# Optimization experiments

Measured on AMD Instinct MI355X. Metric: run time of the kernel, lower is better.

The kernel has to match this reference:

```python
import jax, jax.numpy as jnp
from jax import lax
import numpy as np

N_GROUP = 1024   # number of FPS centroids
N_SAMPLE = 32    # neighbors per ball query
RADIUS = 0.2
BN_EPS = 1e-5    # torch BatchNorm2d default, training-mode batch stats
MLP = [64, 64, 128]
IN_CH = 6        # 3 relative xyz + 3 point features


def setup_inputs() -> dict:
    key = jax.random.key(0)
    ks = jax.random.split(key, 8)
    B, N = 16, 4096
    out = {
        "xyz": jax.random.uniform(ks[0], (B, N, 3), dtype=jnp.float32),
        "point_feature": jax.random.normal(ks[1], (B, N, 3), dtype=jnp.float32),
    }
    last = IN_CH
    for li, oc in enumerate(MLP):
        out[f"w{li}"] = jax.random.normal(ks[2 + li], (oc, last), dtype=jnp.float32) / np.float32(np.sqrt(last))
        out[f"b{li}"] = jnp.zeros((oc,), jnp.float32)
        out[f"g{li}"] = jnp.ones((oc,), jnp.float32)
        out[f"be{li}"] = jnp.zeros((oc,), jnp.float32)
        last = oc
    return out


def _fps(xyz, n_group):
    # Farthest point sampling. xyz: [B, N, 3] -> idx [B, n_group]
    B, N, _ = xyz.shape

    def step(carry, _):
        dist, farthest = carry                      # [B,N], [B]
        centroid = jnp.take_along_axis(xyz, farthest[:, None, None], axis=1)  # [B,1,3]
        d = jnp.sum((xyz - centroid) ** 2, -1)      # [B,N]
        dist = jnp.minimum(dist, d)
        nxt = jnp.argmax(dist, -1).astype(jnp.int32)
        return (dist, nxt), farthest

    init = (jnp.full((B, N), 1e10, xyz.dtype), jnp.zeros((B,), jnp.int32))
    _, idxs = lax.scan(step, init, None, length=n_group)
    return idxs.T                                    # [B, n_group]


def _ball_query(xyz, new_xyz, radius, n_sample):
    # xyz: [B,N,3], new_xyz: [B,S,3] -> idx [B,S,n_sample]
    B, N, _ = xyz.shape
    sqr = jnp.sum((new_xyz[:, :, None, :] - xyz[:, None, :, :]) ** 2, -1)  # [B,S,N]
    idx = jnp.where(sqr > radius * radius, N, jnp.arange(N, dtype=jnp.int32))
    idx = jnp.sort(idx, axis=-1)[:, :, :n_sample]    # closest-index fill like torch impl
    first = idx[:, :, :1]
    return jnp.where(idx == N, first, idx)


def reference(xyz, point_feature, w0, b0, g0, be0, w1, b1, g1, be1, w2, b2, g2, be2):
    B = xyz.shape[0]
    fps_idx = _fps(xyz, N_GROUP)                     # [B,S]
    bi = jnp.arange(B)[:, None]
    new_xyz = xyz[bi, fps_idx]                       # [B,S,3]

    idx = _ball_query(xyz, new_xyz, RADIUS, N_SAMPLE)  # [B,S,K]
    bii = jnp.arange(B)[:, None, None]
    grouped_xyz = xyz[bii, idx] - new_xyz[:, :, None, :]   # [B,S,K,3] centered
    grouped_feat = point_feature[bii, idx]                 # [B,S,K,3]
    x = jnp.concatenate([grouped_xyz, grouped_feat], -1)   # [B,S,K,6]

    # 1x1 Conv2d == per-point linear; BN over all dims but channel (training stats)
    for w, b, g, be in ((w0, b0, g0, be0), (w1, b1, g1, be1), (w2, b2, g2, be2)):
        x = jnp.einsum('bskc,oc->bsko', x, w) + b
        mu = x.mean((0, 1, 2))
        var = x.var((0, 1, 2))
        x = g * (x - mu) * lax.rsqrt(var + BN_EPS) + be
        x = jax.nn.relu(x)

    new_feature = x.max(axis=2)                      # max over n_sample -> [B,S,128]
    return new_xyz, new_feature
```

## Files before the change

### kernel.cpp

```cpp
#include <hip/hip_runtime.h>

constexpr int BATCH = 16;
constexpr int NPT   = 4096;
constexpr int NGRP  = 1024;
constexpr int NSMP  = 32;
constexpr int NPTS  = BATCH * NGRP * NSMP;
constexpr int PBLK  = 4096;
constexpr int NG    = BATCH * NGRP;

__device__ __forceinline__ float sqd(float dx, float dy, float dz) {
  return __fadd_rn(__fadd_rn(__fmul_rn(dx, dx), __fmul_rn(dy, dy)), __fmul_rn(dz, dz));
}

template <int CTRL, int RM>
__device__ __forceinline__ unsigned long long dpp_lvl(unsigned long long P) {
  const int lo = (int)(unsigned int)P;
  const int hi = (int)(unsigned int)(P >> 32);
  const int tlo = __builtin_amdgcn_update_dpp(lo, lo, CTRL, RM, 0xF, false);
  const int thi = __builtin_amdgcn_update_dpp(hi, hi, CTRL, RM, 0xF, false);
  const unsigned long long T =
      ((unsigned long long)(unsigned int)thi << 32) | (unsigned int)tlo;
  return (T > P) ? T : P;
}

__global__ __launch_bounds__(256) void fps_kernel(const float* __restrict__ xyz,
                                                  float* __restrict__ out) {
  __shared__ float sx[NPT], sy[NPT], sz[NPT];
  __shared__ unsigned int ex[2][5][4];
  const int b = blockIdx.x;
  const int t = threadIdx.x;
  const float* src = xyz + (size_t)b * NPT * 3;
  for (int i = t; i < NPT; i += 256) {
    sx[i] = src[i * 3 + 0];
    sy[i] = src[i * 3 + 1];
    sz[i] = src[i * 3 + 2];
  }
  __syncthreads();
  float px[16], py[16], pz[16], dist[16];
  #pragma unroll
  for (int j = 0; j < 16; ++j) {
    const int p = j * 256 + t;
    px[j] = sx[p]; py[j] = sy[p]; pz[j] = sz[p];
    dist[j] = 1e10f;
  }
  const int w = t >> 6;
  float cx = sx[0], cy = sy[0], cz = sz[0];
  float* outx = out + (size_t)b * NGRP * 3;
  for (int step = 0; step < NGRP; ++step) {
    if (t == 0) {
      outx[step * 3 + 0] = cx;
      outx[step * 3 + 1] = cy;
      outx[step * 3 + 2] = cz;
    }
    float bestd = -1.0f; int bestj = 0;
    #pragma unroll
    for (int j = 0; j < 16; ++j) {
      float d = sqd(px[j] - cx, py[j] - cy, pz[j] - cz);
      d = fminf(dist[j], d);
      dist[j] = d;
      if (d > bestd) { bestd = d; bestj = j; }
    }
    const int myidx = bestj * 256 + t;
    const unsigned long long myP =
        ((unsigned long long)__float_as_uint(bestd) << 32) |
        (unsigned long long)(unsigned int)~myidx;
    const float mx = sx[myidx], my_ = sy[myidx], mz = sz[myidx];
    unsigned long long P = myP;
    P = dpp_lvl<0xB1, 0xF>(P);
    P = dpp_lvl<0x4E, 0xF>(P);
    P = dpp_lvl<0x141, 0xF>(P);
    P = dpp_lvl<0x140, 0xF>(P);
    P = dpp_lvl<0x142, 0xA>(P);
    P = dpp_lvl<0x143, 0xC>(P);
    const unsigned int flo = (unsigned int)__builtin_amdgcn_readlane((int)(unsigned int)P, 63);
    const unsigned int fhi =
        (unsigned int)__builtin_amdgcn_readlane((int)(unsigned int)(P >> 32), 63);
    const unsigned long long PF = ((unsigned long long)fhi << 32) | flo;
    const int pb = step & 1;
    if (myP == PF) {
      ex[pb][0][w] = fhi;
      ex[pb][1][w] = flo;
      ex[pb][2][w] = __float_as_uint(mx);
      ex[pb][3][w] = __float_as_uint(my_);
      ex[pb][4][w] = __float_as_uint(mz);
    }
    __syncthreads();
    const unsigned int* e = &ex[pb][0][0];
    unsigned long long best = ((unsigned long long)e[0] << 32) | e[4];
    cx = __uint_as_float(e[8]);
    cy = __uint_as_float(e[12]);
    cz = __uint_as_float(e[16]);
    #pragma unroll
    for (int k = 1; k < 4; ++k) {
      const unsigned long long pk_ = ((unsigned long long)e[k] << 32) | e[4 + k];
      if (pk_ > best) {
        best = pk_;
        cx = __uint_as_float(e[8 + k]);
        cy = __uint_as_float(e[12 + k]);
        cz = __uint_as_float(e[16 + k]);
      }
    }
  }
}

__global__ __launch_bounds__(256) void ballq_kernel(const float* __restrict__ xyz,
                                                    const float* __restrict__ out,
                                                    int* __restrict__ idxg) {
  __shared__ float sx[NPT], sy[NPT], sz[NPT];
  const int b = blockIdx.x >> 4;
  const int sub = blockIdx.x & 15;
  const float* src = xyz + (size_t)b * NPT * 3;
  for (int i = threadIdx.x; i < NPT; i += 256) {
    sx[i] = src[i * 3 + 0];
    sy[i] = src[i * 3 + 1];
    sz[i] = src[i * 3 + 2];
  }
  __syncthreads();
  const int lane = threadIdx.x & 63;
  const int w = threadIdx.x >> 6;
  const float R2 = __fmul_rn(0.2f, 0.2f);
  for (int gi = 0; gi < 16; ++gi) {
    const int s = sub * 64 + w * 16 + gi;
    const float* c = out + ((size_t)b * NGRP + s) * 3;
    const float nx = c[0], ny = c[1], nz = c[2];
    int* og = idxg + ((size_t)b * NGRP + s) * NSMP;
    int cnt = 0, firstP = -1;
    for (int base = 0; base < NPT; base += 64) {
      const int p = base + lane;
      const float dsq = sqd(nx - sx[p], ny - sy[p], nz - sz[p]);
      const bool inr = (dsq <= R2);
      unsigned long long m = __ballot(inr);
      if (firstP < 0 && m) firstP = base + (int)__builtin_ctzll(m);
      const int rank = (int)__popcll(m & ((1ull << lane) - 1ull));
      if (inr) {
        const int pos = cnt + rank;
        if (pos < NSMP) og[pos] = p;
      }
      cnt += (int)__popcll(m);
      if (cnt >= NSMP) break;
    }
    if (cnt < NSMP) {
      for (int pos = cnt + lane; pos < NSMP; pos += 64) og[pos] = firstP;
    }
  }
}

__global__ void transpose_w3(const float* __restrict__ w3, float* __restrict__ w3t) {
  const int i = blockIdx.x * 256 + threadIdx.x;
  if (i < 128 * 64) {
    const int o = i >> 6, c = i & 63;
    w3t[c * 128 + o] = w3[i];
  }
}

__device__ __forceinline__ void gather6(const float* __restrict__ xyz, const float* __restrict__ pf,
                                        const float* __restrict__ nxyz, const int* __restrict__ idxg,
                                        int tid, float in[6]) {
  const int g = tid >> 5;
  const int b = g >> 10;
  const int i = idxg[tid];
  const float* P = xyz + ((size_t)b * NPT + i) * 3;
  const float* C = nxyz + (size_t)g * 3;
  in[0] = P[0] - C[0];
  in[1] = P[1] - C[1];
  in[2] = P[2] - C[2];
  const float* F = pf + ((size_t)b * NPT + i) * 3;
  in[3] = F[0]; in[4] = F[1]; in[5] = F[2];
}

__device__ __forceinline__ void layer1h(const float in[6], const float* __restrict__ w1,
                                        const float* __restrict__ b1, const float* __restrict__ ss1,
                                        float h1[64]) {
  #pragma unroll
  for (int o = 0; o < 64; ++o) {
    float a = b1[o];
    #pragma unroll
    for (int cc = 0; cc < 6; ++cc) a = fmaf(in[cc], w1[o * 6 + cc], a);
    h1[o] = fmaxf(0.0f, fmaf(a, ss1[o], ss1[64 + o]));
  }
}

__device__ __forceinline__ void zb_stats64(const float* zb, float* __restrict__ part,
                                           int chbase, int nch, int t, int blk) {
  const int c = t >> 1, h = t & 1;
  const float* row = zb + c * 129 + h * 64;
  float s = 0.0f, q = 0.0f;
  for (int i = 0; i < 64; ++i) {
    const float v = row[i];
    s += v;
    q = fmaf(v, v, q);
  }
  s += __shfl_xor(s, 1);
  q += __shfl_xor(q, 1);
  if (h == 0) {
    part[(size_t)(chbase + c) * PBLK + blk]       = s;
    part[(size_t)(nch + chbase + c) * PBLK + blk] = q;
  }
}

__device__ __forceinline__ void zb_stats_mm(const float* zb, float* __restrict__ part,
                                            float* __restrict__ pmax, float* __restrict__ pmin,
                                            int chbase, int nch, int t, int blk) {
  const int c = t >> 1, h = t & 1;
  const float* row = zb + c * 129 + h * 64;
  float s = 0.0f, q = 0.0f;
  float mx0 = -3.4e38f, mn0 = 3.4e38f, mx1 = -3.4e38f, mn1 = 3.4e38f;
  for (int i = 0; i < 32; ++i) {
    const float v = row[i];
    s += v; q = fmaf(v, v, q);
    mx0 = fmaxf(mx0, v); mn0 = fminf(mn0, v);
  }
  for (int i = 32; i < 64; ++i) {
    const float v = row[i];
    s += v; q = fmaf(v, v, q);
    mx1 = fmaxf(mx1, v); mn1 = fminf(mn1, v);
  }
  s += __shfl_xor(s, 1);
  q += __shfl_xor(q, 1);
  if (h == 0) {
    part[(size_t)(chbase + c) * PBLK + blk]       = s;
    part[(size_t)(nch + chbase + c) * PBLK + blk] = q;
  }
  const size_t g0 = (size_t)blk * 4 + 2 * h;
  pmax[g0 * 128 + chbase + c]       = mx0;
  pmax[(g0 + 1) * 128 + chbase + c] = mx1;
  pmin[g0 * 128 + chbase + c]       = mn0;
  pmin[(g0 + 1) * 128 + chbase + c] = mn1;
}

__global__ __launch_bounds__(128) void pass1_kernel(const float* __restrict__ xyz, const float* __restrict__ pf,
                                                    const float* __restrict__ nxyz, const int* __restrict__ idxg,
                                                    const float* __restrict__ w1, const float* __restrict__ b1,
                                                    float* __restrict__ part) {
  __shared__ float zb[64 * 129];
  const int t = threadIdx.x;
  const int tid = blockIdx.x * 128 + t;
  float in[6];
  gather6(xyz, pf, nxyz, idxg, tid, in);
  for (int o = 0; o < 64; ++o) {
    float a = b1[o];
    #pragma unroll
    for (int cc = 0; cc < 6; ++cc) a = fmaf(in[cc], w1[o * 6 + cc], a);
    zb[o * 129 + t] = a;
  }
  __syncthreads();
  zb_stats64(zb, part, 0, 64, t, blockIdx.x);
}

__global__ __launch_bounds__(256) void reduce_kernel(const float* __restrict__ part, int nblk, int nch,
                                                     const float* __restrict__ g, const float* __restrict__ be,
                                                     float* __restrict__ ss) {
  const int c = blockIdx.x;
  const int t = threadIdx.x;
  double s = 0.0, q = 0.0;
  for (int i = t; i < nblk; i += 256) {
    s += (double)part[(size_t)c * nblk + i];
    q += (double)part[(size_t)(nch + c) * nblk + i];
  }
  #pragma unroll
  for (int off = 1; off < 64; off <<= 1) {
    s += __shfl_xor(s, off);
    q += __shfl_xor(q, off);
  }
  __shared__ double ls[4], lq[4];
  const int lane = t & 63, w = t >> 6;
  if (lane == 0) { ls[w] = s; lq[w] = q; }
  __syncthreads();
  if (t == 0) {
    const double S = ls[0] + ls[1] + ls[2] + ls[3];
    const double Q = lq[0] + lq[1] + lq[2] + lq[3];
    const double n = (double)NPTS;
    const double mu = S / n;
    const double var = Q / n - mu * mu;
    const double inv = 1.0 / sqrt(var + 1e-5);
    ss[c]       = (float)((double)g[c] * inv);
    ss[nch + c] = (float)((double)be[c] - (double)g[c] * mu * inv);
  }
}

__global__ __launch_bounds__(128) void pass2_kernel(const float* __restrict__ xyz, const float* __restrict__ pf,
                                                    const float* __restrict__ nxyz, const int* __restrict__ idxg,
                                                    const float* __restrict__ w1, const float* __restrict__ b1,
                                                    const float* __restrict__ ss1,
                                                    const float* __restrict__ w2, const float* __restrict__ b2,
                                                    float* __restrict__ part) {
  __shared__ float zb[64 * 129];
  const int t = threadIdx.x;
  const int tid = blockIdx.x * 128 + t;
  float in[6];
  gather6(xyz, pf, nxyz, idxg, tid, in);
  float h1[64];
  layer1h(in, w1, b1, ss1, h1);
  for (int o = 0; o < 64; ++o) {
    float a = b2[o];
    #pragma unroll
    for (int cc = 0; cc < 64; ++cc) a = fmaf(h1[cc], w2[o * 64 + cc], a);
    zb[o * 129 + t] = a;
  }
  __syncthreads();
  zb_stats64(zb, part, 0, 64, t, blockIdx.x);
}

__device__ __forceinline__ void compute_z3(const float* __restrict__ xyz, const float* __restrict__ pf,
                                           const float* __restrict__ nxyz, const int* __restrict__ idxg,
                                           const float* __restrict__ w1, const float* __restrict__ b1,
                                           const float* __restrict__ ss1,
                                           const float* __restrict__ w2, const float* __restrict__ b2,
                                           const float* __restrict__ ss2,
                                           const float* __restrict__ w3t, const float* __restrict__ b3,
                                           float* shm, int t, int tid, float acc[128]) {
  float in[6];
  gather6(xyz, pf, nxyz, idxg, tid, in);
  float h1[64];
  layer1h(in, w1, b1, ss1, h1);
  float* hrow = shm + t * 65;
  for (int o = 0; o < 64; ++o) {
    float a = b2[o];
    #pragma unroll
    for (int cc = 0; cc < 64; ++cc) a = fmaf(h1[cc], w2[o * 64 + cc], a);
    hrow[o] = fmaxf(0.0f, fmaf(a, ss2[o], ss2[64 + o]));
  }
  #pragma unroll
  for (int o = 0; o < 128; ++o) acc[o] = b3[o];
  for (int cc = 0; cc < 64; ++cc) {
    const float hc = hrow[cc];
    const float* wrow = w3t + cc * 128;
    #pragma unroll
    for (int o = 0; o < 128; ++o) acc[o] = fmaf(hc, wrow[o], acc[o]);
  }
}

__global__ __launch_bounds__(128) void pass3_kernel(const float* __restrict__ xyz, const float* __restrict__ pf,
                                                    const float* __restrict__ nxyz, const int* __restrict__ idxg,
                                                    const float* __restrict__ w1, const float* __restrict__ b1,
                                                    const float* __restrict__ ss1,
                                                    const float* __restrict__ w2, const float* __restrict__ b2,
                                                    const float* __restrict__ ss2,
                                                    const float* __restrict__ w3t, const float* __restrict__ b3,
                                                    float* __restrict__ part,
                                                    float* __restrict__ pmax, float* __restrict__ pmin) {
  __shared__ float shm[8320];
  const int t = threadIdx.x;
  const int tid = blockIdx.x * 128 + t;
  float acc[128];
  compute_z3(xyz, pf, nxyz, idxg, w1, b1, ss1, w2, b2, ss2, w3t, b3, shm, t, tid, acc);
  __syncthreads();
  #pragma unroll
  for (int o = 0; o < 64; ++o) shm[o * 129 + t] = acc[o];
  __syncthreads();
  if (pmax) zb_stats_mm(shm, part, pmax, pmin, 0, 128, t, blockIdx.x);
  else      zb_stats64(shm, part, 0, 128, t, blockIdx.x);
  __syncthreads();
  #pragma unroll
  for (int o = 0; o < 64; ++o) shm[o * 129 + t] = acc[64 + o];
  __syncthreads();
  if (pmax) zb_stats_mm(shm, part, pmax, pmin, 64, 128, t, blockIdx.x);
  else      zb_stats64(shm, part, 64, 128, t, blockIdx.x);
}

__global__ __launch_bounds__(256) void pass4f_kernel(const float* __restrict__ pmax,
                                                     const float* __restrict__ pmin,
                                                     const float* __restrict__ ss3,
                                                     float* __restrict__ outF) {
  const int i = blockIdx.x * 256 + threadIdx.x;
  const int c = i & 127;
  const float a = ss3[c], bb = ss3[128 + c];
  const float z = (a >= 0.0f) ? pmax[i] : pmin[i];
  outF[i] = fmaxf(0.0f, fmaf(z, a, bb));
}

__global__ __launch_bounds__(128) void pass4_kernel(const float* __restrict__ xyz, const float* __restrict__ pf,
                                                    const float* __restrict__ nxyz, const int* __restrict__ idxg,
                                                    const float* __restrict__ w1, const float* __restrict__ b1,
                                                    const float* __restrict__ ss1,
                                                    const float* __restrict__ w2, const float* __restrict__ b2,
                                                    const float* __restrict__ ss2,
                                                    const float* __restrict__ w3t, const float* __restrict__ b3,
                                                    const float* __restrict__ ss3,
                                                    float* __restrict__ outF) {
  __shared__ float shm[8320];
  const int t = threadIdx.x;
  const int tid = blockIdx.x * 128 + t;
  float acc[128];
  compute_z3(xyz, pf, nxyz, idxg, w1, b1, ss1, w2, b2, ss2, w3t, b3, shm, t, tid, acc);
  #pragma unroll
  for (int o = 0; o < 128; ++o)
    acc[o] = fmaxf(0.0f, fmaf(acc[o], ss3[o], ss3[128 + o]));
  __syncthreads();
  const int c4 = t & 63, gp = t >> 6;
  #pragma unroll
  for (int o = 0; o < 64; ++o) shm[o * 129 + t] = acc[o];
  __syncthreads();
  #pragma unroll
  for (int gs = 0; gs < 2; ++gs) {
    const int g = gp * 2 + gs;
    const float* row = shm + c4 * 129 + g * 32;
    float m = row[0];
    for (int i = 1; i < 32; ++i) m = fmaxf(m, row[i]);
    outF[((size_t)blockIdx.x * 4 + g) * 128 + c4] = m;
  }
  __syncthreads();
  #pragma unroll
  for (int o = 0; o < 64; ++o) shm[o * 129 + t] = acc[64 + o];
  __syncthreads();
  #pragma unroll
  for (int gs = 0; gs < 2; ++gs) {
    const int g = gp * 2 + gs;
    const float* row = shm + c4 * 129 + g * 32;
    float m = row[0];
    for (int i = 1; i < 32; ++i) m = fmaxf(m, row[i]);
    outF[((size_t)blockIdx.x * 4 + g) * 128 + 64 + c4] = m;
  }
}

extern "C" void kernel_launch(void* const* d_in, const int* in_sizes, int n_in,
                              void* d_out, int out_size, void* d_ws, size_t ws_size,
                              hipStream_t stream) {
  (void)in_sizes; (void)n_in; (void)out_size;
  const float* xyz = (const float*)d_in[0];
  const float* pf  = (const float*)d_in[1];
  const float* w1  = (const float*)d_in[2];
  const float* b1  = (const float*)d_in[3];
  const float* g1  = (const float*)d_in[4];
  const float* be1 = (const float*)d_in[5];
  const float* w2  = (const float*)d_in[6];
  const float* b2  = (const float*)d_in[7];
  const float* g2  = (const float*)d_in[8];
  const float* be2 = (const float*)d_in[9];
  const float* w3  = (const float*)d_in[10];
  const float* b3  = (const float*)d_in[11];
  const float* g3  = (const float*)d_in[12];
  const float* be3 = (const float*)d_in[13];
  float* out = (float*)d_out;

  int*   idxg = (int*)d_ws;
  float* p1   = (float*)((char*)d_ws + (size_t)NPTS * 4);
  float* ss1  = p1 + (size_t)PBLK * 128;
  float* p2   = ss1 + 128;
  float* ss2  = p2 + (size_t)PBLK * 128;
  float* p3   = ss2 + 128;
  float* ss3  = p3 + (size_t)PBLK * 256;
  float* w3t  = ss3 + 256;
  float* pmax = w3t + 8192;
  float* pmin = pmax + (size_t)NG * 128;
  const size_t needed = (size_t)((char*)(pmin + (size_t)NG * 128) - (char*)d_ws);
  const bool fast4 = (ws_size >= needed);

  transpose_w3<<<32, 256, 0, stream>>>(w3, w3t);
  fps_kernel<<<BATCH, 256, 0, stream>>>(xyz, out);
  ballq_kernel<<<BATCH * 16, 256, 0, stream>>>(xyz, out, idxg);
  pass1_kernel<<<PBLK, 128, 0, stream>>>(xyz, pf, out, idxg, w1, b1, p1);
  reduce_kernel<<<64, 256, 0, stream>>>(p1, PBLK, 64, g1, be1, ss1);
  pass2_kernel<<<PBLK, 128, 0, stream>>>(xyz, pf, out, idxg, w1, b1, ss1, w2, b2, p2);
  reduce_kernel<<<64, 256, 0, stream>>>(p2, PBLK, 64, g2, be2, ss2);
  pass3_kernel<<<PBLK, 128, 0, stream>>>(xyz, pf, out, idxg, w1, b1, ss1, w2, b2, ss2, w3t, b3, p3,
                                         fast4 ? pmax : nullptr, fast4 ? pmin : nullptr);
  reduce_kernel<<<128, 256, 0, stream>>>(p3, PBLK, 128, g3, be3, ss3);
  float* outF = out + (size_t)BATCH * NGRP * 3;
  if (fast4) {
    pass4f_kernel<<<(NG * 128) / 256, 256, 0, stream>>>(pmax, pmin, ss3, outF);
  } else {
    pass4_kernel<<<PBLK, 128, 0, stream>>>(xyz, pf, out, idxg, w1, b1, ss1, w2, b2, ss2, w3t, b3, ss3,
                                           outF);
  }
}
```

Before: 1.396 ms.

## Pack two batches per FPS block with 512 threads

The farthest point sampling kernel now processes two batch items per 512-thread block, each half using its own shared-memory point arrays and exchange buffers, and launches half as many blocks. A single __syncthreads now couples both halves at every step, so each batch's serial loop waits on the other. This halves the block count on a kernel that already used only 16 blocks, which seems aimed at per-block or per-CU latency effects, but it also puts two batches on one CU and adds cross-batch barrier coupling.

New measurement: 1.735 ms. 24.3% more time.

```diff
diff --git a/kernel.cpp b/kernel.cpp
--- a/kernel.cpp
+++ b/kernel.cpp
@@ -23,28 +23,29 @@
   return (T > P) ? T : P;
 }
 
-__global__ __launch_bounds__(256) void fps_kernel(const float* __restrict__ xyz,
+__global__ __launch_bounds__(512) void fps_kernel(const float* __restrict__ xyz,
                                                   float* __restrict__ out) {
-  __shared__ float sx[NPT], sy[NPT], sz[NPT];
-  __shared__ unsigned int ex[2][5][4];
-  const int b = blockIdx.x;
-  const int t = threadIdx.x;
+  __shared__ float sx[2][NPT], sy[2][NPT], sz[2][NPT];
+  __shared__ unsigned int ex[2][2][5][4];
+  const int sub = threadIdx.x >> 8;
+  const int t = threadIdx.x & 255;
+  const int b = blockIdx.x * 2 + sub;
   const float* src = xyz + (size_t)b * NPT * 3;
   for (int i = t; i < NPT; i += 256) {
-    sx[i] = src[i * 3 + 0];
-    sy[i] = src[i * 3 + 1];
-    sz[i] = src[i * 3 + 2];
+    sx[sub][i] = src[i * 3 + 0];
+    sy[sub][i] = src[i * 3 + 1];
+    sz[sub][i] = src[i * 3 + 2];
   }
   __syncthreads();
   float px[16], py[16], pz[16], dist[16];
   #pragma unroll
   for (int j = 0; j < 16; ++j) {
     const int p = j * 256 + t;
-    px[j] = sx[p]; py[j] = sy[p]; pz[j] = sz[p];
+    px[j] = sx[sub][p]; py[j] = sy[sub][p]; pz[j] = sz[sub][p];
     dist[j] = 1e10f;
   }
-  const int w = t >> 6;
-  float cx = sx[0], cy = sy[0], cz = sz[0];
+  const int w = (threadIdx.x >> 6) & 3;
+  float cx = sx[sub][0], cy = sy[sub][0], cz = sz[sub][0];
   float* outx = out + (size_t)b * NGRP * 3;
   for (int step = 0; step < NGRP; ++step) {
     if (t == 0) {
@@ -64,7 +65,7 @@
     const unsigned long long myP =
         ((unsigned long long)__float_as_uint(bestd) << 32) |
         (unsigned long long)(unsigned int)~myidx;
-    const float mx = sx[myidx], my_ = sy[myidx], mz = sz[myidx];
+    const float mx = sx[sub][myidx], my_ = sy[sub][myidx], mz = sz[sub][myidx];
     unsigned long long P = myP;
     P = dpp_lvl<0xB1, 0xF>(P);
     P = dpp_lvl<0x4E, 0xF>(P);
@@ -78,14 +79,14 @@
     const unsigned long long PF = ((unsigned long long)fhi << 32) | flo;
     const int pb = step & 1;
     if (myP == PF) {
-      ex[pb][0][w] = fhi;
-      ex[pb][1][w] = flo;
-      ex[pb][2][w] = __float_as_uint(mx);
-      ex[pb][3][w] = __float_as_uint(my_);
-      ex[pb][4][w] = __float_as_uint(mz);
+      ex[sub][pb][0][w] = fhi;
+      ex[sub][pb][1][w] = flo;
+      ex[sub][pb][2][w] = __float_as_uint(mx);
+      ex[sub][pb][3][w] = __float_as_uint(my_);
+      ex[sub][pb][4][w] = __float_as_uint(mz);
     }
     __syncthreads();
-    const unsigned int* e = &ex[pb][0][0];
+    const unsigned int* e = &ex[sub][pb][0][0];
     unsigned long long best = ((unsigned long long)e[0] << 32) | e[4];
     cx = __uint_as_float(e[8]);
     cy = __uint_as_float(e[12]);
@@ -447,7 +448,7 @@
   const bool fast4 = (ws_size >= needed);
 
   transpose_w3<<<32, 256, 0, stream>>>(w3, w3t);
-  fps_kernel<<<BATCH, 256, 0, stream>>>(xyz, out);
+  fps_kernel<<<BATCH / 2, 512, 0, stream>>>(xyz, out);
   ballq_kernel<<<BATCH * 16, 256, 0, stream>>>(xyz, out, idxg);
   pass1_kernel<<<PBLK, 128, 0, stream>>>(xyz, pf, out, idxg, w1, b1, p1);
   reduce_kernel<<<64, 256, 0, stream>>>(p1, PBLK, 64, g1, be1, ss1);
```

## Compute layer-1 BN stats from input moments; tree-reduce FPS argmax

Applied to the files above, without the earlier changes.

Layer-1 batch-norm statistics are now derived analytically from the first and second moments of the 6-channel grouped input (6 sums plus 21 cross products), finalized in double precision with the weights. This replaces materializing 64 channel outputs per point and reducing them. Separately, the FPS per-thread argmax over 16 registers becomes a pairwise tree of selects instead of a serial compare chain, which shortens the per-step dependency chain. Float accumulation of second moments followed by mean subtraction risks cancellation, and the single-block finalize adds a serial reduction over 4096 partials.

After: 1.704 ms. 22.0% more time.

```diff
diff --git a/kernel.cpp b/kernel.cpp
--- a/kernel.cpp
+++ b/kernel.cpp
@@ -52,14 +52,38 @@
       outx[step * 3 + 1] = cy;
       outx[step * 3 + 2] = cz;
     }
-    float bestd = -1.0f; int bestj = 0;
+    float d[16];
     #pragma unroll
     for (int j = 0; j < 16; ++j) {
-      float d = sqd(px[j] - cx, py[j] - cy, pz[j] - cz);
-      d = fminf(dist[j], d);
-      dist[j] = d;
-      if (d > bestd) { bestd = d; bestj = j; }
-    }
+      float dd = sqd(px[j] - cx, py[j] - cy, pz[j] - cz);
+      dd = fminf(dist[j], dd);
+      dist[j] = dd;
+      d[j] = dd;
+    }
+    float v0[8]; int i0[8];
+    #pragma unroll
+    for (int k = 0; k < 8; ++k) {
+      const bool g = d[2 * k + 1] > d[2 * k];
+      v0[k] = g ? d[2 * k + 1] : d[2 * k];
+      i0[k] = g ? 2 * k + 1 : 2 * k;
+    }
+    float v1[4]; int i1[4];
+    #pragma unroll
+    for (int k = 0; k < 4; ++k) {
+      const bool g = v0[2 * k + 1] > v0[2 * k];
+      v1[k] = g ? v0[2 * k + 1] : v0[2 * k];
+      i1[k] = g ? i0[2 * k + 1] : i0[2 * k];
+    }
+    float v2[2]; int i2[2];
+    #pragma unroll
+    for (int k = 0; k < 2; ++k) {
+      const bool g = v1[2 * k + 1] > v1[2 * k];
+      v2[k] = g ? v1[2 * k + 1] : v1[2 * k];
+      i2[k] = g ? i1[2 * k + 1] : i1[2 * k];
+    }
+    const bool gf = v2[1] > v2[0];
+    const float bestd = gf ? v2[1] : v2[0];
+    const int bestj = gf ? i2[1] : i2[0];
     const int myidx = bestj * 256 + t;
     const unsigned long long myP =
         ((unsigned long long)__float_as_uint(bestd) << 32) |
@@ -228,23 +252,80 @@
   pmin[(g0 + 1) * 128 + chbase + c] = mn1;
 }
 
-__global__ __launch_bounds__(128) void pass1_kernel(const float* __restrict__ xyz, const float* __restrict__ pf,
-                                                    const float* __restrict__ nxyz, const int* __restrict__ idxg,
-                                                    const float* __restrict__ w1, const float* __restrict__ b1,
-                                                    float* __restrict__ part) {
-  __shared__ float zb[64 * 129];
-  const int t = threadIdx.x;
-  const int tid = blockIdx.x * 128 + t;
-  float in[6];
-  gather6(xyz, pf, nxyz, idxg, tid, in);
-  for (int o = 0; o < 64; ++o) {
-    float a = b1[o];
-    #pragma unroll
-    for (int cc = 0; cc < 6; ++cc) a = fmaf(in[cc], w1[o * 6 + cc], a);
-    zb[o * 129 + t] = a;
-  }
-  __syncthreads();
-  zb_stats64(zb, part, 0, 64, t, blockIdx.x);
+__global__ __launch_bounds__(256) void mom1_kernel(const float* __restrict__ xyz,
+                                                   const float* __restrict__ pf,
+                                                   const float* __restrict__ nxyz,
+                                                   const int* __restrict__ idxg,
+                                                   float* __restrict__ part) {
+  const int t = threadIdx.x;
+  const int base = blockIdx.x * 512 + t;
+  float acc[27];
+  #pragma unroll
+  for (int k = 0; k < 27; ++k) acc[k] = 0.0f;
+  #pragma unroll
+  for (int pp = 0; pp < 2; ++pp) {
+    float in[6];
+    gather6(xyz, pf, nxyz, idxg, base + pp * 256, in);
+    #pragma unroll
+    for (int i = 0; i < 6; ++i) acc[i] += in[i];
+    int k = 6;
+    #pragma unroll
+    for (int i = 0; i < 6; ++i)
+      #pragma unroll
+      for (int j = i; j < 6; ++j) { acc[k] = fmaf(in[i], in[j], acc[k]); ++k; }
+  }
+  #pragma unroll
+  for (int off = 1; off < 64; off <<= 1) {
+    #pragma unroll
+    for (int k = 0; k < 27; ++k) acc[k] += __shfl_xor(acc[k], off);
+  }
+  const int lane = t & 63, w = t >> 6;
+  if (lane == 0) {
+    const int slot = blockIdx.x * 4 + w;
+    #pragma unroll
+    for (int k = 0; k < 27; ++k) part[k * 4096 + slot] = acc[k];
+  }
+}
+
+__global__ __launch_bounds__(64) void finalize1_kernel(const float* __restrict__ part,
+                                                       const float* __restrict__ w1,
+                                                       const float* __restrict__ b1,
+                                                       const float* __restrict__ g,
+                                                       const float* __restrict__ be,
+                                                       float* __restrict__ ss) {
+  __shared__ double sm[27];
+  const int t = threadIdx.x;
+  if (t < 27) {
+    double s = 0.0;
+    #pragma unroll 4
+    for (int i = 0; i < 4096; ++i) s += (double)part[t * 4096 + i];
+    sm[t] = s;
+  }
+  __syncthreads();
+  const double N = (double)NPTS;
+  double wv[6];
+  #pragma unroll
+  for (int i = 0; i < 6; ++i) wv[i] = (double)w1[t * 6 + i];
+  double mean_wx = 0.0;
+  #pragma unroll
+  for (int i = 0; i < 6; ++i) mean_wx += wv[i] * sm[i];
+  mean_wx /= N;
+  const double bb = (double)b1[t];
+  const double mu = mean_wx + bb;
+  double qq = 0.0;
+  int k = 6;
+  #pragma unroll
+  for (int i = 0; i < 6; ++i)
+    #pragma unroll
+    for (int j = i; j < 6; ++j) {
+      qq += (i == j ? 1.0 : 2.0) * wv[i] * wv[j] * (sm[k] / N);
+      ++k;
+    }
+  const double Ez2 = qq + 2.0 * bb * mean_wx + bb * bb;
+  const double var = Ez2 - mu * mu;
+  const double inv = 1.0 / sqrt(var + 1e-5);
+  ss[t]      = (float)((double)g[t] * inv);
+  ss[64 + t] = (float)((double)be[t] - (double)g[t] * mu * inv);
 }
 
 __global__ __launch_bounds__(256) void reduce_kernel(const float* __restrict__ part, int nblk, int nch,
@@ -449,8 +530,8 @@
   transpose_w3<<<32, 256, 0, stream>>>(w3, w3t);
   fps_kernel<<<BATCH, 256, 0, stream>>>(xyz, out);
   ballq_kernel<<<BATCH * 16, 256, 0, stream>>>(xyz, out, idxg);
-  pass1_kernel<<<PBLK, 128, 0, stream>>>(xyz, pf, out, idxg, w1, b1, p1);
-  reduce_kernel<<<64, 256, 0, stream>>>(p1, PBLK, 64, g1, be1, ss1);
+  mom1_kernel<<<1024, 256, 0, stream>>>(xyz, pf, out, idxg, p1);
+  finalize1_kernel<<<1, 64, 0, stream>>>(p1, w1, b1, g1, be1, ss1);
   pass2_kernel<<<PBLK, 128, 0, stream>>>(xyz, pf, out, idxg, w1, b1, ss1, w2, b2, p2);
   reduce_kernel<<<64, 256, 0, stream>>>(p2, PBLK, 64, g2, be2, ss2);
   pass3_kernel<<<PBLK, 128, 0, stream>>>(xyz, pf, out, idxg, w1, b1, ss1, w2, b2, ss2, w3t, b3, p3,
```
